# Optimization experiments

Measured on AMD Instinct MI355X. Metric: run time of the kernel, lower is better.

The kernel has to match this reference:

```python
import jax, jax.numpy as jnp
import numpy as np

CH = 512
NUM_HEADS = 8
NUM_GROUPS = 32  # min(32, channels)
EPS = 1e-5


def setup_inputs() -> dict:
    key = jax.random.key(0)
    ks = jax.random.split(key, 4)
    B, C, H, W = 8, CH, 32, 32
    x = jax.random.normal(ks[0], (B, C, H, W), dtype=jnp.float32)
    gn_weight = jnp.ones((C,), dtype=jnp.float32)
    gn_bias = jnp.zeros((C,), dtype=jnp.float32)
    # 1x1 conv weights stored as [out_ch, in_ch] (kernel dims squeezed)
    qkv_weight = jax.random.normal(ks[1], (3 * C, C), dtype=jnp.float32) * (C ** -0.5)
    qkv_bias = jnp.zeros((3 * C,), dtype=jnp.float32)
    proj_weight = jax.random.normal(ks[2], (C, C), dtype=jnp.float32) * (C ** -0.5)
    proj_bias = jnp.zeros((C,), dtype=jnp.float32)
    return {
        "x": x,
        "gn_weight": gn_weight,
        "gn_bias": gn_bias,
        "qkv_weight": qkv_weight,
        "qkv_bias": qkv_bias,
        "proj_weight": proj_weight,
        "proj_bias": proj_bias,
    }


def _group_norm(x, weight, bias):
    B, C, H, W = x.shape
    g = x.reshape(B, NUM_GROUPS, C // NUM_GROUPS, H, W)
    mean = jnp.mean(g, axis=(2, 3, 4), keepdims=True)
    var = jnp.var(g, axis=(2, 3, 4), keepdims=True)
    g = (g - mean) * jax.lax.rsqrt(var + EPS)
    g = g.reshape(B, C, H, W)
    return g * weight[None, :, None, None] + bias[None, :, None, None]


def reference(x, gn_weight, gn_bias, qkv_weight, qkv_bias, proj_weight, proj_bias):
    B, C, H, W = x.shape
    nh = NUM_HEADS
    hc = C // nh
    N = H * W

    h = _group_norm(x, gn_weight, gn_bias)
    # 1x1 conv == per-pixel matmul
    qkv = jnp.einsum('oc,bchw->bohw', qkv_weight, h) + qkv_bias[None, :, None, None]
    q, k, v = jnp.split(qkv, 3, axis=1)
    # b (h c) x y -> b h c (x y)
    q = q.reshape(B, nh, hc, N)
    k = k.reshape(B, nh, hc, N)
    v = v.reshape(B, nh, hc, N)

    scale = hc ** -0.5
    attn = jnp.einsum('bhci,bhcj->bhij', q, k) * scale  # [B, nh, N, N]
    attn = jax.nn.softmax(attn, axis=-1)
    out = jnp.einsum('bhij,bhcj->bhci', attn, v)  # [B, nh, hc, N]
    out = out.reshape(B, C, H, W)
    out = jnp.einsum('oc,bchw->bohw', proj_weight, out) + proj_bias[None, :, None, None]
    return x + out
```

## Files before the change

kernel.cpp:

```cpp
#include <hip/hip_runtime.h>
#include <math.h>

#define B_   8
#define C_   512
#define N_   1024
#define NH_  8
#define HC_  64

typedef __attribute__((ext_vector_type(8))) short bf16x8;
typedef __attribute__((ext_vector_type(4))) float f32x4;

#define MFMA16(a, b, c) __builtin_amdgcn_mfma_f32_16x16x32_bf16(a, b, c, 0, 0, 0)

__device__ __forceinline__ unsigned short f2bf(float f) {
  unsigned u = __builtin_bit_cast(unsigned, f);
  u += 0x7fffu + ((u >> 16) & 1u);
  return (unsigned short)(u >> 16);
}

__device__ __forceinline__ unsigned pack2(float a, float b) {
  return (unsigned)f2bf(a) | ((unsigned)f2bf(b) << 16);
}

__device__ __forceinline__ void gll16(const void* g, void* l) {
  __builtin_amdgcn_global_load_lds(
      (const __attribute__((address_space(1))) unsigned int*)g,
      (__attribute__((address_space(3))) unsigned int*)l, 16, 0, 0);
}

__global__ __launch_bounds__(256) void prep(const float* __restrict__ x,
                                            const float* __restrict__ gw,
                                            const float* __restrict__ gb,
                                            const float* __restrict__ qkvw,
                                            const float* __restrict__ pw,
                                            unsigned short* __restrict__ hT,
                                            unsigned short* __restrict__ qkvw_bf,
                                            unsigned short* __restrict__ projw_bf) {
  const int t = threadIdx.x;
  if (blockIdx.x >= 256) {
    const int widx = blockIdx.x - 256;
    const float* src = (widx < 768) ? qkvw : pw;
    unsigned short* dst = (widx < 768) ? qkvw_bf : projw_bf;
    const int i = ((widx < 768) ? widx : widx - 768) * 1024 + t * 4;
    const float4 v = *(const float4*)(src + i);
    ushort4 o;
    o.x = f2bf(v.x); o.y = f2bf(v.y); o.z = f2bf(v.z); o.w = f2bf(v.w);
    *(ushort4*)(dst + i) = o;
    return;
  }
  const int b = blockIdx.x >> 5;
  const int g = blockIdx.x & 31;
  const float* xg = x + ((size_t)b * C_ + (size_t)g * 16) * N_;

  float4 xv[16];
  float s = 0.f, ss = 0.f;
#pragma unroll
  for (int k = 0; k < 16; ++k) {
    xv[k] = *(const float4*)(xg + (size_t)k * N_ + t * 4);
    s  += xv[k].x + xv[k].y + xv[k].z + xv[k].w;
    ss += xv[k].x * xv[k].x + xv[k].y * xv[k].y + xv[k].z * xv[k].z + xv[k].w * xv[k].w;
  }
#pragma unroll
  for (int off = 32; off > 0; off >>= 1) {
    s  += __shfl_down(s, off);
    ss += __shfl_down(ss, off);
  }
  __shared__ float rs[4], rss[4], sh_mi[2];
  if ((t & 63) == 0) { rs[t >> 6] = s; rss[t >> 6] = ss; }
  __syncthreads();
  if (t == 0) {
    s  = rs[0] + rs[1] + rs[2] + rs[3];
    ss = rss[0] + rss[1] + rss[2] + rss[3];
    const float mean = s * (1.f / 16384.f);
    const float var  = ss * (1.f / 16384.f) - mean * mean;
    sh_mi[0] = mean;
    sh_mi[1] = rsqrtf(var + 1e-5f);
  }
  __syncthreads();
  const float mean = sh_mi[0], inv = sh_mi[1];

  float sc[16], of[16];
#pragma unroll
  for (int k = 0; k < 16; ++k) {
    const int c = g * 16 + k;
    sc[k] = inv * gw[c];
    of[k] = gb[c] - mean * sc[k];
  }
#pragma unroll
  for (int r = 0; r < 4; ++r) {
    const int p = t * 4 + r;
    unsigned short* dst = hT + ((size_t)b * N_ + p) * C_ + g * 16;
    uint4 o0, o1;
    const float* f0 = (const float*)&xv[0];
#pragma unroll
    for (int k2 = 0; k2 < 4; ++k2) {
      const float a0 = ((const float*)&xv[k2 * 2 + 0])[r] * sc[k2 * 2 + 0] + of[k2 * 2 + 0];
      const float a1 = ((const float*)&xv[k2 * 2 + 1])[r] * sc[k2 * 2 + 1] + of[k2 * 2 + 1];
      ((unsigned*)&o0)[k2] = pack2(a0, a1);
      const float b0 = ((const float*)&xv[8 + k2 * 2 + 0])[r] * sc[8 + k2 * 2 + 0] + of[8 + k2 * 2 + 0];
      const float b1 = ((const float*)&xv[8 + k2 * 2 + 1])[r] * sc[8 + k2 * 2 + 1] + of[8 + k2 * 2 + 1];
      ((unsigned*)&o1)[k2] = pack2(b0, b1);
    }
    (void)f0;
    *(uint4*)(dst)     = o0;
    *(uint4*)(dst + 8) = o1;
  }
}

__global__ __launch_bounds__(256, 3) void gemm_qkv(
    const unsigned short* __restrict__ A, const float* __restrict__ bias,
    const unsigned short* __restrict__ BT, unsigned short* __restrict__ qkTout,
    unsigned short* __restrict__ vout) {
  __shared__ __attribute__((aligned(16))) short lds[16 * 512];
  const int t = threadIdx.x;
  const int lane = t & 63, w = t >> 6;
  const int lm = lane & 15, q = lane >> 4;
  const int wm = w >> 1, wn = w & 1;
  const int b = blockIdx.z;
  const int m0 = blockIdx.y * 128, n0 = blockIdx.x * 128;
  const unsigned short* Bb = BT + (size_t)b * N_ * C_;

  f32x4 acc[4][4];
#pragma unroll
  for (int i = 0; i < 4; ++i)
#pragma unroll
    for (int j = 0; j < 4; ++j) acc[i][j] = (f32x4){0.f, 0.f, 0.f, 0.f};

  for (int k0 = 0; k0 < C_; k0 += 32) {
    __syncthreads();
#pragma unroll
    for (int ff = 0; ff < 2; ++ff) {
      const int f = w * 2 + ff;
      gll16(A  + (size_t)(m0 + f * 16 + lm) * C_ + k0 + q * 8, lds + f * 512);
      gll16(Bb + (size_t)(n0 + f * 16 + lm) * C_ + k0 + q * 8, lds + (8 + f) * 512);
    }
    __syncthreads();
    bf16x8 af[4], bf[4];
#pragma unroll
    for (int mi = 0; mi < 4; ++mi)
      af[mi] = *(const bf16x8*)(lds + (wm * 4 + mi) * 512 + lane * 8);
#pragma unroll
    for (int ni = 0; ni < 4; ++ni)
      bf[ni] = *(const bf16x8*)(lds + (8 + wn * 4 + ni) * 512 + lane * 8);
#pragma unroll
    for (int mi = 0; mi < 4; ++mi)
#pragma unroll
      for (int ni = 0; ni < 4; ++ni)
        acc[mi][ni] = MFMA16(af[mi], bf[ni], acc[mi][ni]);
  }

  if (blockIdx.y < 8) {
    const bool isQ = (blockIdx.y < 4);
#pragma unroll
    for (int mi = 0; mi < 4; ++mi) {
#pragma unroll
      for (int ni = 0; ni < 4; ++ni) {
        const int col  = n0 + wn * 64 + ni * 16 + lm;
        const int row0 = m0 + wm * 64 + mi * 16 + q * 4;
        float v0 = acc[mi][ni][0] + bias[row0 + 0];
        float v1 = acc[mi][ni][1] + bias[row0 + 1];
        float v2 = acc[mi][ni][2] + bias[row0 + 2];
        float v3 = acc[mi][ni][3] + bias[row0 + 3];
        if (isQ) { v0 *= 0.125f; v1 *= 0.125f; v2 *= 0.125f; v3 *= 0.125f; }
        ushort4 o4;
        o4.x = f2bf(v0); o4.y = f2bf(v1); o4.z = f2bf(v2); o4.w = f2bf(v3);
        *(ushort4*)&qkTout[((size_t)b * N_ + col) * 1024 + row0] = o4;
      }
    }
  } else {
#pragma unroll
    for (int mi = 0; mi < 4; ++mi)
#pragma unroll
      for (int ni = 0; ni < 4; ++ni) {
        const int col = n0 + wn * 64 + ni * 16 + lm;
#pragma unroll
        for (int r = 0; r < 4; ++r) {
          const int row = m0 + wm * 64 + mi * 16 + q * 4 + r;
          vout[((size_t)b * 512 + row - 1024) * N_ + col] =
              f2bf(acc[mi][ni][r] + bias[row]);
        }
      }
  }
}

__global__ __launch_bounds__(256, 2) void gemm_proj(
    const unsigned short* __restrict__ A, const float* __restrict__ bias,
    const unsigned short* __restrict__ BT, const float* __restrict__ resid,
    float* __restrict__ outf) {
  __shared__ __attribute__((aligned(16))) short lds[12 * 512];
  const int t = threadIdx.x;
  const int lane = t & 63, w = t >> 6;
  const int lm = lane & 15, q = lane >> 4;
  const int wm = w >> 1, wn = w & 1;
  const int b = blockIdx.z;
  const int m0 = blockIdx.y * 128, n0 = blockIdx.x * 64;
  const unsigned short* Bb = BT + (size_t)b * N_ * C_;

  f32x4 acc[4][2];
#pragma unroll
  for (int i = 0; i < 4; ++i)
#pragma unroll
    for (int j = 0; j < 2; ++j) acc[i][j] = (f32x4){0.f, 0.f, 0.f, 0.f};

  for (int k0 = 0; k0 < C_; k0 += 32) {
    __syncthreads();
#pragma unroll
    for (int ff = 0; ff < 2; ++ff) {
      const int f = w * 2 + ff;
      gll16(A + (size_t)(m0 + f * 16 + lm) * C_ + k0 + q * 8, lds + f * 512);
    }
    gll16(Bb + (size_t)(n0 + w * 16 + lm) * C_ + k0 + q * 8, lds + (8 + w) * 512);
    __syncthreads();
    bf16x8 af[4], bf[2];
#pragma unroll
    for (int mi = 0; mi < 4; ++mi)
      af[mi] = *(const bf16x8*)(lds + (wm * 4 + mi) * 512 + lane * 8);
#pragma unroll
    for (int ni = 0; ni < 2; ++ni)
      bf[ni] = *(const bf16x8*)(lds + (8 + wn * 2 + ni) * 512 + lane * 8);
#pragma unroll
    for (int mi = 0; mi < 4; ++mi)
#pragma unroll
      for (int ni = 0; ni < 2; ++ni)
        acc[mi][ni] = MFMA16(af[mi], bf[ni], acc[mi][ni]);
  }

#pragma unroll
  for (int mi = 0; mi < 4; ++mi)
#pragma unroll
    for (int ni = 0; ni < 2; ++ni) {
      const int col = n0 + wn * 32 + ni * 16 + lm;
#pragma unroll
      for (int r = 0; r < 4; ++r) {
        const int row = m0 + wm * 64 + mi * 16 + q * 4 + r;
        const size_t oi = ((size_t)b * 512 + row) * N_ + col;
        outf[oi] = acc[mi][ni][r] + bias[row] + resid[oi];
      }
    }
}

__global__ __launch_bounds__(256, 4) void attn_mfma(
    const unsigned short* __restrict__ qkT, const unsigned short* __restrict__ vbuf,
    unsigned short* __restrict__ aoT) {
  __shared__ __attribute__((aligned(16))) short lds[32 * 512];
  short* Qb = lds;
  short* Kb = lds + 8 * 512;
  short* Vb = lds + 16 * 512;
  short* Pb = lds + 24 * 512;

  const int t = threadIdx.x;
  const int lane = t & 63, w = t >> 6;
  const int lm = lane & 15, q = lane >> 4;
  const int i0 = blockIdx.x * 64;
  const int hh = blockIdx.y;
  const int b = blockIdx.z;

  const unsigned short* QT = qkT + (size_t)b * N_ * 1024;
  const unsigned short* Vp = vbuf + ((size_t)b * 512 + hh * 64) * N_;

#pragma unroll
  for (int ff = 0; ff < 2; ++ff)
    gll16(QT + (size_t)(i0 + w * 16 + lm) * 1024 + hh * 64 + ff * 32 + q * 8,
          Qb + (w * 2 + ff) * 512);
  __syncthreads();

  bf16x8 af[2];
#pragma unroll
  for (int ks = 0; ks < 2; ++ks)
    af[ks] = *(const bf16x8*)(Qb + (w * 2 + ks) * 512 + lane * 8);

  f32x4 accO[4], lrun = (f32x4){0.f, 0.f, 0.f, 0.f};
#pragma unroll
  for (int nc = 0; nc < 4; ++nc) accO[nc] = (f32x4){0.f, 0.f, 0.f, 0.f};

  for (int jt = 0; jt < 16; ++jt) {
    const int j0 = jt * 64;
    __syncthreads();
#pragma unroll
    for (int ks = 0; ks < 2; ++ks) {
      gll16(QT + (size_t)(j0 + w * 16 + lm) * 1024 + 512 + hh * 64 + ks * 32 + q * 8,
            Kb + (w * 2 + ks) * 512);
      gll16(Vp + (size_t)(w * 16 + lm) * N_ + j0 + ks * 32 + q * 8,
            Vb + (w * 2 + ks) * 512);
    }
    __syncthreads();

    f32x4 accS[4];
#pragma unroll
    for (int nj = 0; nj < 4; ++nj) accS[nj] = (f32x4){0.f, 0.f, 0.f, 0.f};
#pragma unroll
    for (int nj = 0; nj < 4; ++nj)
#pragma unroll
      for (int ks = 0; ks < 2; ++ks) {
        const bf16x8 bfr = *(const bf16x8*)(Kb + (nj * 2 + ks) * 512 + lane * 8);
        accS[nj] = MFMA16(af[ks], bfr, accS[nj]);
      }

#pragma unroll
    for (int nj = 0; nj < 4; ++nj)
#pragma unroll
      for (int r = 0; r < 4; ++r) {
        const float p = __expf(accS[nj][r]);
        accS[nj][r] = p;
        lrun[r] += p;
      }
#pragma unroll
    for (int nj = 0; nj < 4; ++nj) {
      const int jin = nj * 16 + lm;
      const int ks = jin >> 5;
      const int qt = (jin >> 3) & 3;
      const int jp = jin & 7;
      short* pp = Pb + (w * 2 + ks) * 512 + qt * 128 + jp;
#pragma unroll
      for (int r = 0; r < 4; ++r)
        pp[(q * 4 + r) * 8] = (short)f2bf(accS[nj][r]);
    }

#pragma unroll
    for (int ks = 0; ks < 2; ++ks) {
      const bf16x8 pf = *(const bf16x8*)(Pb + (w * 2 + ks) * 512 + lane * 8);
#pragma unroll
      for (int nc = 0; nc < 4; ++nc) {
        const bf16x8 vf = *(const bf16x8*)(Vb + (nc * 2 + ks) * 512 + lane * 8);
        accO[nc] = MFMA16(pf, vf, accO[nc]);
      }
    }
  }

#pragma unroll
  for (int d = 1; d <= 8; d <<= 1)
#pragma unroll
    for (int r = 0; r < 4; ++r) lrun[r] += __shfl_xor(lrun[r], d);
  f32x4 linv;
#pragma unroll
  for (int r = 0; r < 4; ++r) linv[r] = 1.f / lrun[r];

  unsigned short* aob = aoT + (size_t)b * N_ * C_;
#pragma unroll
  for (int nc = 0; nc < 4; ++nc) {
    const int col = hh * 64 + nc * 16 + lm;
#pragma unroll
    for (int r = 0; r < 4; ++r) {
      const int i = i0 + w * 16 + q * 4 + r;
      aob[(size_t)i * C_ + col] = f2bf(accO[nc][r] * linv[r]);
    }
  }
}

extern "C" void kernel_launch(void* const* d_in, const int* in_sizes, int n_in,
                              void* d_out, int out_size, void* d_ws, size_t ws_size,
                              hipStream_t stream) {
  const float* x    = (const float*)d_in[0];
  const float* gw   = (const float*)d_in[1];
  const float* gb   = (const float*)d_in[2];
  const float* qkvw = (const float*)d_in[3];
  const float* qkvb = (const float*)d_in[4];
  const float* pw   = (const float*)d_in[5];
  const float* pb   = (const float*)d_in[6];
  float* out = (float*)d_out;

  unsigned short* hT       = (unsigned short*)d_ws;
  unsigned short* qkvw_bf  = hT + (size_t)B_ * N_ * C_;
  unsigned short* projw_bf = qkvw_bf + 1536 * 512;
  unsigned short* qkT      = projw_bf + 512 * 512;
  unsigned short* vbuf     = qkT + (size_t)B_ * N_ * 1024;
  unsigned short* aoTp     = vbuf + (size_t)B_ * 512 * N_;

  prep<<<1280, 256, 0, stream>>>(x, gw, gb, qkvw, pw, hT, qkvw_bf, projw_bf);
  gemm_qkv<<<dim3(8, 12, B_), 256, 0, stream>>>(qkvw_bf, qkvb, hT, qkT, vbuf);
  attn_mfma<<<dim3(16, NH_, B_), 256, 0, stream>>>(qkT, vbuf, aoTp);
  gemm_proj<<<dim3(16, 4, B_), 256, 0, stream>>>(projw_bf, pb, aoTp, x, out);
}
```

Before: 166.9 us.

## Deepen GEMM K-step, stage epilogues through LDS for coalesced stores, truncate P

Both GEMMs now load a 64-wide K slice per barrier pair instead of 32, halving the number of synchronizations per tile. The QKV GEMM and attention epilogues write results into padded LDS tiles and then emit 16-byte coalesced global stores instead of scattered 2- or 8-byte writes. The softmax probabilities are converted to bf16 by truncation rather than round-to-nearest, which slightly reduces accuracy. The larger LDS footprint in gemm_qkv (about 34 KB) may lower occupancy.

```diff
diff --git a/kernel.cpp b/kernel.cpp
--- a/kernel.cpp
+++ b/kernel.cpp
@@ -16,6 +16,10 @@
   unsigned u = __builtin_bit_cast(unsigned, f);
   u += 0x7fffu + ((u >> 16) & 1u);
   return (unsigned short)(u >> 16);
+}
+
+__device__ __forceinline__ unsigned short f2bf_trunc(float f) {
+  return (unsigned short)(__builtin_bit_cast(unsigned, f) >> 16);
 }
 
 __device__ __forceinline__ unsigned pack2(float a, float b) {
@@ -91,7 +95,6 @@
     const int p = t * 4 + r;
     unsigned short* dst = hT + ((size_t)b * N_ + p) * C_ + g * 16;
     uint4 o0, o1;
-    const float* f0 = (const float*)&xv[0];
 #pragma unroll
     for (int k2 = 0; k2 < 4; ++k2) {
       const float a0 = ((const float*)&xv[k2 * 2 + 0])[r] * sc[k2 * 2 + 0] + of[k2 * 2 + 0];
@@ -101,7 +104,6 @@
       const float b1 = ((const float*)&xv[8 + k2 * 2 + 1])[r] * sc[8 + k2 * 2 + 1] + of[8 + k2 * 2 + 1];
       ((unsigned*)&o1)[k2] = pack2(b0, b1);
     }
-    (void)f0;
     *(uint4*)(dst)     = o0;
     *(uint4*)(dst + 8) = o1;
   }
@@ -111,7 +113,7 @@
     const unsigned short* __restrict__ A, const float* __restrict__ bias,
     const unsigned short* __restrict__ BT, unsigned short* __restrict__ qkTout,
     unsigned short* __restrict__ vout) {
-  __shared__ __attribute__((aligned(16))) short lds[16 * 512];
+  __shared__ __attribute__((aligned(16))) short lds[128 * 136];
   const int t = threadIdx.x;
   const int lane = t & 63, w = t >> 6;
   const int lm = lane & 15, q = lane >> 4;
@@ -126,60 +128,84 @@
 #pragma unroll
     for (int j = 0; j < 4; ++j) acc[i][j] = (f32x4){0.f, 0.f, 0.f, 0.f};
 
-  for (int k0 = 0; k0 < C_; k0 += 32) {
-    __syncthreads();
-#pragma unroll
-    for (int ff = 0; ff < 2; ++ff) {
-      const int f = w * 2 + ff;
-      gll16(A  + (size_t)(m0 + f * 16 + lm) * C_ + k0 + q * 8, lds + f * 512);
-      gll16(Bb + (size_t)(n0 + f * 16 + lm) * C_ + k0 + q * 8, lds + (8 + f) * 512);
-    }
-    __syncthreads();
-    bf16x8 af[4], bf[4];
+  for (int k0 = 0; k0 < C_; k0 += 64) {
+    __syncthreads();
+#pragma unroll
+    for (int rr = 0; rr < 2; ++rr) {
+      const int rg = w * 2 + rr;
+#pragma unroll
+      for (int ks = 0; ks < 2; ++ks) {
+        gll16(A  + (size_t)(m0 + rg * 16 + lm) * C_ + k0 + ks * 32 + q * 8,
+              lds + (rg * 2 + ks) * 512);
+        gll16(Bb + (size_t)(n0 + rg * 16 + lm) * C_ + k0 + ks * 32 + q * 8,
+              lds + (16 + rg * 2 + ks) * 512);
+      }
+    }
+    __syncthreads();
+    bf16x8 af[4][2];
 #pragma unroll
     for (int mi = 0; mi < 4; ++mi)
-      af[mi] = *(const bf16x8*)(lds + (wm * 4 + mi) * 512 + lane * 8);
+#pragma unroll
+      for (int ks = 0; ks < 2; ++ks)
+        af[mi][ks] = *(const bf16x8*)(lds + (((wm * 4 + mi) * 2) + ks) * 512 + lane * 8);
 #pragma unroll
     for (int ni = 0; ni < 4; ++ni)
-      bf[ni] = *(const bf16x8*)(lds + (8 + wn * 4 + ni) * 512 + lane * 8);
+#pragma unroll
+      for (int ks = 0; ks < 2; ++ks) {
+        const bf16x8 bfr =
+            *(const bf16x8*)(lds + (16 + ((wn * 4 + ni) * 2) + ks) * 512 + lane * 8);
+#pragma unroll
+        for (int mi = 0; mi < 4; ++mi)
+          acc[mi][ni] = MFMA16(af[mi][ks], bfr, acc[mi][ni]);
+      }
+  }
+
+  __syncthreads();
+  if (blockIdx.y < 8) {
+    const float qs = (blockIdx.y < 4) ? 0.125f : 1.0f;
+#pragma unroll
+    for (int mi = 0; mi < 4; ++mi) {
+#pragma unroll
+      for (int ni = 0; ni < 4; ++ni) {
+        const int pl = wn * 64 + ni * 16 + lm;
+        const int ol0 = wm * 64 + mi * 16 + q * 4;
+        ushort4 o4;
+        o4.x = f2bf((acc[mi][ni][0] + bias[m0 + ol0 + 0]) * qs);
+        o4.y = f2bf((acc[mi][ni][1] + bias[m0 + ol0 + 1]) * qs);
+        o4.z = f2bf((acc[mi][ni][2] + bias[m0 + ol0 + 2]) * qs);
+        o4.w = f2bf((acc[mi][ni][3] + bias[m0 + ol0 + 3]) * qs);
+        *(ushort4*)&lds[pl * 136 + ol0] = o4;
+      }
+    }
+    __syncthreads();
+#pragma unroll
+    for (int u = 0; u < 8; ++u) {
+      const int flat = u * 256 + t;
+      const int oc = flat & 15, pl = flat >> 4;
+      *(uint4*)&qkTout[((size_t)b * N_ + n0 + pl) * 1024 + m0 + oc * 8] =
+          *(const uint4*)&lds[pl * 136 + oc * 8];
+    }
+  } else {
 #pragma unroll
     for (int mi = 0; mi < 4; ++mi)
 #pragma unroll
-      for (int ni = 0; ni < 4; ++ni)
-        acc[mi][ni] = MFMA16(af[mi], bf[ni], acc[mi][ni]);
-  }
-
-  if (blockIdx.y < 8) {
-    const bool isQ = (blockIdx.y < 4);
-#pragma unroll
-    for (int mi = 0; mi < 4; ++mi) {
-#pragma unroll
       for (int ni = 0; ni < 4; ++ni) {
-        const int col  = n0 + wn * 64 + ni * 16 + lm;
-        const int row0 = m0 + wm * 64 + mi * 16 + q * 4;
-        float v0 = acc[mi][ni][0] + bias[row0 + 0];
-        float v1 = acc[mi][ni][1] + bias[row0 + 1];
-        float v2 = acc[mi][ni][2] + bias[row0 + 2];
-        float v3 = acc[mi][ni][3] + bias[row0 + 3];
-        if (isQ) { v0 *= 0.125f; v1 *= 0.125f; v2 *= 0.125f; v3 *= 0.125f; }
-        ushort4 o4;
-        o4.x = f2bf(v0); o4.y = f2bf(v1); o4.z = f2bf(v2); o4.w = f2bf(v3);
-        *(ushort4*)&qkTout[((size_t)b * N_ + col) * 1024 + row0] = o4;
-      }
-    }
-  } else {
-#pragma unroll
-    for (int mi = 0; mi < 4; ++mi)
-#pragma unroll
-      for (int ni = 0; ni < 4; ++ni) {
-        const int col = n0 + wn * 64 + ni * 16 + lm;
+        const int pl = wn * 64 + ni * 16 + lm;
 #pragma unroll
         for (int r = 0; r < 4; ++r) {
-          const int row = m0 + wm * 64 + mi * 16 + q * 4 + r;
-          vout[((size_t)b * 512 + row - 1024) * N_ + col] =
-              f2bf(acc[mi][ni][r] + bias[row]);
+          const int ol = wm * 64 + mi * 16 + q * 4 + r;
+          lds[ol * 136 + pl] = f2bf(acc[mi][ni][r] + bias[m0 + ol]);
         }
       }
+    __syncthreads();
+    const int c0 = m0 - 1024;
+#pragma unroll
+    for (int u = 0; u < 8; ++u) {
+      const int flat = u * 256 + t;
+      const int pc = flat & 15, ol = flat >> 4;
+      *(uint4*)&vout[((size_t)b * 512 + c0 + ol) * N_ + n0 + pc * 8] =
+          *(const uint4*)&lds[ol * 136 + pc * 8];
+    }
   }
 }
 
@@ -187,7 +213,7 @@
     const unsigned short* __restrict__ A, const float* __restrict__ bias,
     const unsigned short* __restrict__ BT, const float* __restrict__ resid,
     float* __restrict__ outf) {
-  __shared__ __attribute__((aligned(16))) short lds[12 * 512];
+  __shared__ __attribute__((aligned(16))) short lds[24 * 512];
   const int t = threadIdx.x;
   const int lane = t & 63, w = t >> 6;
   const int lm = lane & 15, q = lane >> 4;
@@ -202,27 +228,37 @@
 #pragma unroll
     for (int j = 0; j < 2; ++j) acc[i][j] = (f32x4){0.f, 0.f, 0.f, 0.f};
 
-  for (int k0 = 0; k0 < C_; k0 += 32) {
-    __syncthreads();
-#pragma unroll
-    for (int ff = 0; ff < 2; ++ff) {
-      const int f = w * 2 + ff;
-      gll16(A + (size_t)(m0 + f * 16 + lm) * C_ + k0 + q * 8, lds + f * 512);
-    }
-    gll16(Bb + (size_t)(n0 + w * 16 + lm) * C_ + k0 + q * 8, lds + (8 + w) * 512);
-    __syncthreads();
-    bf16x8 af[4], bf[2];
+  for (int k0 = 0; k0 < C_; k0 += 64) {
+    __syncthreads();
+#pragma unroll
+    for (int rr = 0; rr < 2; ++rr) {
+      const int rg = w * 2 + rr;
+#pragma unroll
+      for (int ks = 0; ks < 2; ++ks)
+        gll16(A + (size_t)(m0 + rg * 16 + lm) * C_ + k0 + ks * 32 + q * 8,
+              lds + (rg * 2 + ks) * 512);
+    }
+#pragma unroll
+    for (int ks = 0; ks < 2; ++ks)
+      gll16(Bb + (size_t)(n0 + w * 16 + lm) * C_ + k0 + ks * 32 + q * 8,
+            lds + (16 + w * 2 + ks) * 512);
+    __syncthreads();
+    bf16x8 af[4][2];
 #pragma unroll
     for (int mi = 0; mi < 4; ++mi)
-      af[mi] = *(const bf16x8*)(lds + (wm * 4 + mi) * 512 + lane * 8);
+#pragma unroll
+      for (int ks = 0; ks < 2; ++ks)
+        af[mi][ks] = *(const bf16x8*)(lds + (((wm * 4 + mi) * 2) + ks) * 512 + lane * 8);
 #pragma unroll
     for (int ni = 0; ni < 2; ++ni)
-      bf[ni] = *(const bf16x8*)(lds + (8 + wn * 2 + ni) * 512 + lane * 8);
-#pragma unroll
-    for (int mi = 0; mi < 4; ++mi)
-#pragma unroll
-      for (int ni = 0; ni < 2; ++ni)
-        acc[mi][ni] = MFMA16(af[mi], bf[ni], acc[mi][ni]);
+#pragma unroll
+      for (int ks = 0; ks < 2; ++ks) {
+        const bf16x8 bfr =
+            *(const bf16x8*)(lds + (16 + ((wn * 2 + ni) * 2) + ks) * 512 + lane * 8);
+#pragma unroll
+        for (int mi = 0; mi < 4; ++mi)
+          acc[mi][ni] = MFMA16(af[mi][ks], bfr, acc[mi][ni]);
+      }
   }
 
 #pragma unroll
@@ -313,7 +349,7 @@
       short* pp = Pb + (w * 2 + ks) * 512 + qt * 128 + jp;
 #pragma unroll
       for (int r = 0; r < 4; ++r)
-        pp[(q * 4 + r) * 8] = (short)f2bf(accS[nj][r]);
+        pp[(q * 4 + r) * 8] = (short)f2bf_trunc(accS[nj][r]);
     }
 
 #pragma unroll
@@ -335,15 +371,20 @@
 #pragma unroll
   for (int r = 0; r < 4; ++r) linv[r] = 1.f / lrun[r];
 
+  __syncthreads();
+  short* Ep = lds + w * 1152;
+#pragma unroll
+  for (int nc = 0; nc < 4; ++nc)
+#pragma unroll
+    for (int r = 0; r < 4; ++r)
+      Ep[(q * 4 + r) * 72 + nc * 16 + lm] = f2bf(accO[nc][r] * linv[r]);
   unsigned short* aob = aoT + (size_t)b * N_ * C_;
 #pragma unroll
-  for (int nc = 0; nc < 4; ++nc) {
-    const int col = hh * 64 + nc * 16 + lm;
-#pragma unroll
-    for (int r = 0; r < 4; ++r) {
-      const int i = i0 + w * 16 + q * 4 + r;
-      aob[(size_t)i * C_ + col] = f2bf(accO[nc][r] * linv[r]);
-    }
+  for (int u = 0; u < 2; ++u) {
+    const int flat = u * 64 + lane;
+    const int c8 = flat & 7, i = flat >> 3;
+    *(uint4*)&aob[(size_t)(i0 + w * 16 + i) * C_ + hh * 64 + c8 * 8] =
+        *(const uint4*)&Ep[i * 72 + c8 * 8];
   }
 }
 
```

Measured after the change: 165.7 us. Within noise of the previous version (-0.7%).
